# Kernel optimization log

Hardware: AMD Instinct MI355X
Metric: run time of the kernel (lower is better)

## Reference

```python
import jax, jax.numpy as jnp
import numpy as np

EPS = 1e-8
LAM = 0.7  # resonance_lambda


def phase_resonance(a, b, eps=EPS):
    # a, b: (B, N, D) float32. Pairwise phase coherence -> (B, N, N)
    D = a.shape[-1]
    pairs = (D // 2)
    a2 = a[..., :pairs * 2].reshape(*a.shape[:-1], pairs, 2)
    b2 = b[..., :pairs * 2].reshape(*b.shape[:-1], pairs, 2)
    theta_a = jnp.arctan2(a2[..., 1] + eps, a2[..., 0] + eps)  # (B,N,pairs)
    theta_b = jnp.arctan2(b2[..., 1] + eps, b2[..., 0] + eps)  # (B,N,pairs)
    delta = theta_a[:, :, None, :] - theta_b[:, None, :, :]    # (B,N,N,pairs)
    return jnp.cos(delta).mean(axis=-1)                        # (B,N,N)


def setup_inputs() -> dict:
    key = jax.random.key(0)
    k1, k2, k3, k4, k5 = jax.random.split(key, 5)
    B, N, D = 2, 1024, 128
    node_states = jax.random.normal(k1, (B, N, D), dtype=jnp.float32)
    node_gates = jax.random.uniform(k2, (B, N, 1), dtype=jnp.float32)
    r_acc = jax.random.normal(k3, (B, N, N), dtype=jnp.float32)
    # nn.Linear(D, D, bias=False) weights, y = x @ W.T
    scale = 1.0 / np.sqrt(D)
    W_in = jax.random.uniform(k4, (D, D), dtype=jnp.float32, minval=-scale, maxval=scale)
    W_out = jax.random.uniform(k5, (D, D), dtype=jnp.float32, minval=-scale, maxval=scale)
    conductance = jnp.asarray(1.0, dtype=jnp.float32)
    return {"node_states": node_states, "node_gates": node_gates, "r_acc": r_acc,
            "W_in": W_in, "W_out": W_out, "conductance": conductance}


def reference(node_states, node_gates, r_acc, W_in, W_out, conductance):
    B, N, D = node_states.shape
    h = node_states @ W_in.T                                   # field_in projection
    r_instant = phase_resonance(h, h)                          # (B,N,N)
    r_acc_new = LAM * r_acc + (1.0 - LAM) * r_instant
    r_acc_new = jnp.clip(r_acc_new, -2.0, 2.0)
    cond = jnp.clip(conductance, -5.0, 5.0)
    coupling = jax.nn.sigmoid(cond * r_acc_new)                # (B,N,N)
    eye = jnp.eye(N, dtype=coupling.dtype)[None]               # zero self-coupling
    coupling = coupling * (1.0 - eye)
    coupling = coupling * jnp.swapaxes(node_gates, -1, -2)     # (B,1,N) col gates
    coupling = coupling * node_gates                           # (B,N,1) row gates
    coupling = coupling / (coupling.sum(axis=-1, keepdims=True) + 1e-8)
    transmitted = node_states * node_gates
    values = transmitted @ W_out.T                             # field_out projection
    field_signal = coupling @ values                           # (B,N,D)
    return field_signal, r_acc_new
```

## Files before the change

### kernel.cpp

```cpp
#include <hip/hip_runtime.h>
#include <hip/hip_bf16.h>

using bf16x8 = __attribute__((ext_vector_type(8))) short;
using f32x4  = __attribute__((ext_vector_type(4))) float;

#define NN 1024
#define DD 128

__global__ void init_kernel(float* __restrict__ rowsum) {
    int i = blockIdx.x * 256 + threadIdx.x;
    if (i < 2 * NN) rowsum[i] = 0.0f;
}

__global__ __launch_bounds__(256) void prep_kernel(
    const float* __restrict__ states, const float* __restrict__ gates,
    const float* __restrict__ W_in, const float* __restrict__ W_out,
    __hip_bfloat16* __restrict__ M_bf, __hip_bfloat16* __restrict__ valT)
{
    __shared__ float s_state[4 * 128];
    __shared__ float s_WinT[32 * 129];
    __shared__ float s_WoutT[32 * 129];
    __shared__ float s_g[4];

    const int tid = threadIdx.x;
    const int b  = blockIdx.x >> 8;
    const int n0 = (blockIdx.x & 255) * 4;

    const float* sb = states + ((size_t)b * NN + n0) * DD;
    if (tid < 128) ((float4*)s_state)[tid] = ((const float4*)sb)[tid];
    if (tid < 4)   s_g[tid] = gates[b * NN + n0 + tid];

    const int c  = tid & 127;
    const int rg = tid >> 7;
    float acc_h[2] = {0.f, 0.f};
    float acc_v[2] = {0.f, 0.f};

    const int kk = tid & 31;
    const int dg = tid >> 5;
    for (int k0 = 0; k0 < 128; k0 += 32) {
        __syncthreads();
        #pragma unroll
        for (int dd = 0; dd < 16; ++dd) {
            int d = dg * 16 + dd;
            s_WinT [kk * 129 + d] = W_in [d * 128 + k0 + kk];
            s_WoutT[kk * 129 + d] = W_out[d * 128 + k0 + kk];
        }
        __syncthreads();
        #pragma unroll
        for (int k2 = 0; k2 < 32; ++k2) {
            float w1 = s_WinT [k2 * 129 + c];
            float w2 = s_WoutT[k2 * 129 + c];
            #pragma unroll
            for (int r = 0; r < 2; ++r) {
                float s = s_state[(rg * 2 + r) * 128 + k0 + k2];
                acc_h[r] = fmaf(s, w1, acc_h[r]);
                acc_v[r] = fmaf(s, w2, acc_v[r]);
            }
        }
    }

    #pragma unroll
    for (int r = 0; r < 2; ++r) {
        int row = rg * 2 + r;
        float hm = acc_h[r] + 1e-8f;
        float hp = __shfl_xor(hm, 1);
        float x = (c & 1) ? hp : hm;
        float y = (c & 1) ? hm : hp;
        float r2 = x * x + y * y;
        float out;
        if (r2 > 0.f) out = ((c & 1) ? y : x) * rsqrtf(r2);
        else          out = (c & 1) ? 0.f : 1.f;
        M_bf[((size_t)b * NN + n0 + row) * DD + c] = __float2bfloat16(out);
        valT[((size_t)b * DD + c) * NN + n0 + row] = __float2bfloat16(acc_v[r] * s_g[row]);
    }
}

__global__ __launch_bounds__(256) void resonance_kernel(
    const __hip_bfloat16* __restrict__ M_bf,
    const float* __restrict__ r_acc,
    const float* __restrict__ gates,
    const float* __restrict__ cond_ptr,
    float* __restrict__ r_out,
    __hip_bfloat16* __restrict__ c_bf,
    float* __restrict__ rowsum)
{
    const int tid = threadIdx.x;
    const int l  = tid & 63;
    const int w  = tid >> 6;
    const int j0 = blockIdx.x * 32;
    const int i0 = blockIdx.y * 64;
    const int b  = blockIdx.z;

    const int row_a = l & 15;
    const int kg    = l >> 4;

    const bf16x8* Mv = (const bf16x8*)(M_bf + (size_t)b * NN * DD);

    f32x4 acc[2];
    #pragma unroll
    for (int cp = 0; cp < 2; ++cp) acc[cp] = (f32x4){0.f, 0.f, 0.f, 0.f};

    #pragma unroll
    for (int ks = 0; ks < 4; ++ks) {
        int kv = ks * 4 + kg;
        bf16x8 a = Mv[(size_t)(i0 + w * 16 + row_a) * 16 + kv];
        #pragma unroll
        for (int cp = 0; cp < 2; ++cp) {
            bf16x8 bb = Mv[(size_t)(j0 + cp * 16 + row_a) * 16 + kv];
            acc[cp] = __builtin_amdgcn_mfma_f32_16x16x32_bf16(a, bb, acc[cp], 0, 0, 0);
        }
    }

    float cond = fminf(fmaxf(cond_ptr[0], -5.f), 5.f);
    const int i_base = i0 + w * 16 + kg * 4;

    float g_j[2], g_i[4];
    #pragma unroll
    for (int cp = 0; cp < 2; ++cp) g_j[cp] = gates[b * NN + j0 + cp * 16 + row_a];
    #pragma unroll
    for (int q = 0; q < 4; ++q)    g_i[q]  = gates[b * NN + i_base + q];

    const size_t robase = (size_t)b * NN * NN;
    float rs[4] = {0.f, 0.f, 0.f, 0.f};

    #pragma unroll
    for (int q = 0; q < 4; ++q) {
        int i = i_base + q;
        float gi = g_i[q];
        #pragma unroll
        for (int cp = 0; cp < 2; ++cp) {
            int j = j0 + cp * 16 + row_a;
            float s  = acc[cp][q] * (1.f / 64.f);
            float ra = r_acc[robase + (size_t)i * NN + j];
            float rn = fminf(fmaxf(0.7f * ra + 0.3f * s, -2.f), 2.f);
            r_out[robase + (size_t)i * NN + j] = rn;
            float cpl = (i == j) ? 0.f
                        : (1.f / (1.f + __expf(-cond * rn))) * gi * g_j[cp];
            c_bf[robase + (size_t)i * NN + j] = __float2bfloat16(cpl);
            rs[q] += cpl;
        }
    }

    #pragma unroll
    for (int q = 0; q < 4; ++q) {
        float v = rs[q];
        v += __shfl_xor(v, 1);
        v += __shfl_xor(v, 2);
        v += __shfl_xor(v, 4);
        v += __shfl_xor(v, 8);
        if ((l & 15) == 0) atomicAdd(&rowsum[b * NN + i_base + q], v);
    }
}

__global__ __launch_bounds__(256) void gather_kernel(
    const __hip_bfloat16* __restrict__ c_bf,
    const __hip_bfloat16* __restrict__ valT,
    __hip_bfloat16* __restrict__ part)
{
    const int tid = threadIdx.x;
    const int l  = tid & 63;
    const int w  = tid >> 6;
    const int jc = blockIdx.x;
    const int i0 = blockIdx.y * 64;
    const int b  = blockIdx.z;

    const int row_a = l & 15;
    const int kg    = l >> 4;

    const bf16x8* Cv = (const bf16x8*)(c_bf + (size_t)b * NN * NN);
    const bf16x8* Vv = (const bf16x8*)(valT + (size_t)b * DD * NN);

    f32x4 acc[8];
    #pragma unroll
    for (int dt = 0; dt < 8; ++dt) acc[dt] = (f32x4){0.f, 0.f, 0.f, 0.f};

    #pragma unroll
    for (int s = 0; s < 2; ++s) {
        int kv = jc * 8 + s * 4 + kg;
        bf16x8 a = Cv[(size_t)(i0 + w * 16 + row_a) * (NN / 8) + kv];
        #pragma unroll
        for (int dt = 0; dt < 8; ++dt) {
            bf16x8 bb = Vv[(size_t)(dt * 16 + row_a) * (NN / 8) + kv];
            acc[dt] = __builtin_amdgcn_mfma_f32_16x16x32_bf16(a, bb, acc[dt], 0, 0, 0);
        }
    }

    __hip_bfloat16* pb = part + ((size_t)jc * 2 + b) * NN * DD;
    #pragma unroll
    for (int dt = 0; dt < 8; ++dt) {
        #pragma unroll
        for (int q = 0; q < 4; ++q) {
            int i = i0 + w * 16 + kg * 4 + q;
            int d = dt * 16 + row_a;
            pb[(size_t)i * DD + d] = __float2bfloat16(acc[dt][q]);
        }
    }
}

__global__ __launch_bounds__(256) void reduce_kernel(
    const __hip_bfloat16* __restrict__ part,
    const float* __restrict__ rowsum,
    float* __restrict__ field)
{
    int p   = blockIdx.x * 256 + threadIdx.x;
    int b   = p >> 16;
    int rem = p & 65535;
    int i   = rem >> 6;
    int d2  = (rem & 63) * 2;
    size_t base = ((size_t)b * NN + i) * DD + d2;

    float s0 = 0.f, s1 = 0.f;
    #pragma unroll
    for (int jc = 0; jc < 16; ++jc) {
        unsigned int u = *(const unsigned int*)(part + (size_t)jc * 2 * NN * DD + base);
        s0 += __uint_as_float(u << 16);
        s1 += __uint_as_float(u & 0xffff0000u);
    }
    float inv = 1.0f / (rowsum[b * NN + i] + 1e-8f);
    float2 o = {s0 * inv, s1 * inv};
    *(float2*)(field + base) = o;
}

extern "C" void kernel_launch(void* const* d_in, const int* in_sizes, int n_in,
                              void* d_out, int out_size, void* d_ws, size_t ws_size,
                              hipStream_t stream) {
    const float* states = (const float*)d_in[0];
    const float* gates  = (const float*)d_in[1];
    const float* r_acc  = (const float*)d_in[2];
    const float* W_in   = (const float*)d_in[3];
    const float* W_out  = (const float*)d_in[4];
    const float* cond   = (const float*)d_in[5];

    float* field = (float*)d_out;
    float* r_out = field + 2 * NN * DD;

    char* ws = (char*)d_ws;
    __hip_bfloat16* M_bf   = (__hip_bfloat16*)ws;
    __hip_bfloat16* valT   = (__hip_bfloat16*)(ws + (512 << 10));
    __hip_bfloat16* c_bf   = (__hip_bfloat16*)(ws + (1 << 20));
    float*          rowsum = (float*)(ws + (5 << 20));
    __hip_bfloat16* part   = (__hip_bfloat16*)(ws + (6 << 20));

    hipLaunchKernelGGL(init_kernel, dim3(8), dim3(256), 0, stream, rowsum);
    hipLaunchKernelGGL(prep_kernel, dim3(512), dim3(256), 0, stream,
                       states, gates, W_in, W_out, M_bf, valT);
    hipLaunchKernelGGL(resonance_kernel, dim3(32, 16, 2), dim3(256), 0, stream,
                       M_bf, r_acc, gates, cond, r_out, c_bf, rowsum);
    hipLaunchKernelGGL(gather_kernel, dim3(16, 16, 2), dim3(256), 0, stream,
                       c_bf, valT, part);
    hipLaunchKernelGGL(reduce_kernel, dim3(512), dim3(256), 0, stream,
                       part, rowsum, field);
}
```

Baseline: 110.6 us.

## Fuse resonance and gather kernels via shared-memory coupling tile, drop atomics

```diff
diff --git a/kernel.cpp b/kernel.cpp
--- a/kernel.cpp
+++ b/kernel.cpp
@@ -2,14 +2,15 @@
 #include <hip/hip_bf16.h>
 
 using bf16x8 = __attribute__((ext_vector_type(8))) short;
+using bf16x4 = __attribute__((ext_vector_type(4))) short;
 using f32x4  = __attribute__((ext_vector_type(4))) float;
 
 #define NN 1024
 #define DD 128
 
-__global__ void init_kernel(float* __restrict__ rowsum) {
-    int i = blockIdx.x * 256 + threadIdx.x;
-    if (i < 2 * NN) rowsum[i] = 0.0f;
+__device__ __forceinline__ short bf16bits(float f) {
+    __hip_bfloat16 t = __float2bfloat16(f);
+    return *(short*)&t;
 }
 
 __global__ __launch_bounds__(256) void prep_kernel(
@@ -20,6 +21,7 @@
     __shared__ float s_state[4 * 128];
     __shared__ float s_WinT[32 * 129];
     __shared__ float s_WoutT[32 * 129];
+    __shared__ float s_v[4][128];
     __shared__ float s_g[4];
 
     const int tid = threadIdx.x;
@@ -35,15 +37,23 @@
     float acc_h[2] = {0.f, 0.f};
     float acc_v[2] = {0.f, 0.f};
 
-    const int kk = tid & 31;
-    const int dg = tid >> 5;
+    const int kq = tid & 7;
+    const int dl = tid >> 3;
     for (int k0 = 0; k0 < 128; k0 += 32) {
         __syncthreads();
         #pragma unroll
-        for (int dd = 0; dd < 16; ++dd) {
-            int d = dg * 16 + dd;
-            s_WinT [kk * 129 + d] = W_in [d * 128 + k0 + kk];
-            s_WoutT[kk * 129 + d] = W_out[d * 128 + k0 + kk];
+        for (int dp = 0; dp < 4; ++dp) {
+            int d = dp * 32 + dl;
+            float4 w1 = *(const float4*)(W_in  + d * 128 + k0 + kq * 4);
+            float4 w2 = *(const float4*)(W_out + d * 128 + k0 + kq * 4);
+            s_WinT [(kq * 4 + 0) * 129 + d] = w1.x;
+            s_WinT [(kq * 4 + 1) * 129 + d] = w1.y;
+            s_WinT [(kq * 4 + 2) * 129 + d] = w1.z;
+            s_WinT [(kq * 4 + 3) * 129 + d] = w1.w;
+            s_WoutT[(kq * 4 + 0) * 129 + d] = w2.x;
+            s_WoutT[(kq * 4 + 1) * 129 + d] = w2.y;
+            s_WoutT[(kq * 4 + 2) * 129 + d] = w2.z;
+            s_WoutT[(kq * 4 + 3) * 129 + d] = w2.w;
         }
         __syncthreads();
         #pragma unroll
@@ -71,52 +81,67 @@
         if (r2 > 0.f) out = ((c & 1) ? y : x) * rsqrtf(r2);
         else          out = (c & 1) ? 0.f : 1.f;
         M_bf[((size_t)b * NN + n0 + row) * DD + c] = __float2bfloat16(out);
-        valT[((size_t)b * DD + c) * NN + n0 + row] = __float2bfloat16(acc_v[r] * s_g[row]);
-    }
-}
-
-__global__ __launch_bounds__(256) void resonance_kernel(
+        s_v[row][c] = acc_v[r] * s_g[row];
+    }
+    __syncthreads();
+
+    if (tid < 128) {
+        bf16x4 pk;
+        #pragma unroll
+        for (int r = 0; r < 4; ++r) pk[r] = bf16bits(s_v[r][tid]);
+        *(bf16x4*)(valT + ((size_t)b * DD + tid) * NN + n0) = pk;
+    }
+}
+
+__global__ __launch_bounds__(256) void fused_kernel(
     const __hip_bfloat16* __restrict__ M_bf,
+    const __hip_bfloat16* __restrict__ valT,
     const float* __restrict__ r_acc,
     const float* __restrict__ gates,
     const float* __restrict__ cond_ptr,
     float* __restrict__ r_out,
-    __hip_bfloat16* __restrict__ c_bf,
-    float* __restrict__ rowsum)
+    __hip_bfloat16* __restrict__ part,
+    float* __restrict__ part_rs)
 {
+    __shared__ __align__(16) __hip_bfloat16 s_cpl[2][16][72];
+    __shared__ float s_rs[32][2];
+
     const int tid = threadIdx.x;
     const int l  = tid & 63;
     const int w  = tid >> 6;
-    const int j0 = blockIdx.x * 32;
-    const int i0 = blockIdx.y * 64;
-    const int b  = blockIdx.z;
-
+    const int wi = w & 1;
+    const int wj = w >> 1;
     const int row_a = l & 15;
     const int kg    = l >> 4;
 
+    const int jt = blockIdx.x;
+    const int j0 = jt * 64;
+    const int i0 = blockIdx.y * 32;
+    const int b  = blockIdx.z;
+
     const bf16x8* Mv = (const bf16x8*)(M_bf + (size_t)b * NN * DD);
+    const bf16x8* Vv = (const bf16x8*)(valT + (size_t)b * DD * NN);
 
     f32x4 acc[2];
-    #pragma unroll
-    for (int cp = 0; cp < 2; ++cp) acc[cp] = (f32x4){0.f, 0.f, 0.f, 0.f};
-
+    acc[0] = (f32x4){0.f, 0.f, 0.f, 0.f};
+    acc[1] = (f32x4){0.f, 0.f, 0.f, 0.f};
     #pragma unroll
     for (int ks = 0; ks < 4; ++ks) {
         int kv = ks * 4 + kg;
-        bf16x8 a = Mv[(size_t)(i0 + w * 16 + row_a) * 16 + kv];
+        bf16x8 a = Mv[(size_t)(i0 + wi * 16 + row_a) * 16 + kv];
         #pragma unroll
         for (int cp = 0; cp < 2; ++cp) {
-            bf16x8 bb = Mv[(size_t)(j0 + cp * 16 + row_a) * 16 + kv];
+            bf16x8 bb = Mv[(size_t)(j0 + wj * 32 + cp * 16 + row_a) * 16 + kv];
             acc[cp] = __builtin_amdgcn_mfma_f32_16x16x32_bf16(a, bb, acc[cp], 0, 0, 0);
         }
     }
 
     float cond = fminf(fmaxf(cond_ptr[0], -5.f), 5.f);
-    const int i_base = i0 + w * 16 + kg * 4;
+    const int i_base = i0 + wi * 16 + kg * 4;
 
     float g_j[2], g_i[4];
     #pragma unroll
-    for (int cp = 0; cp < 2; ++cp) g_j[cp] = gates[b * NN + j0 + cp * 16 + row_a];
+    for (int cp = 0; cp < 2; ++cp) g_j[cp] = gates[b * NN + j0 + wj * 32 + cp * 16 + row_a];
     #pragma unroll
     for (int q = 0; q < 4; ++q)    g_i[q]  = gates[b * NN + i_base + q];
 
@@ -129,15 +154,16 @@
         float gi = g_i[q];
         #pragma unroll
         for (int cp = 0; cp < 2; ++cp) {
-            int j = j0 + cp * 16 + row_a;
+            int jl = wj * 32 + cp * 16 + row_a;
+            int j  = j0 + jl;
             float s  = acc[cp][q] * (1.f / 64.f);
             float ra = r_acc[robase + (size_t)i * NN + j];
             float rn = fminf(fmaxf(0.7f * ra + 0.3f * s, -2.f), 2.f);
             r_out[robase + (size_t)i * NN + j] = rn;
             float cpl = (i == j) ? 0.f
                         : (1.f / (1.f + __expf(-cond * rn))) * gi * g_j[cp];
-            c_bf[robase + (size_t)i * NN + j] = __float2bfloat16(cpl);
             rs[q] += cpl;
+            s_cpl[wi][kg * 4 + q][jl] = __float2bfloat16(cpl);
         }
     }
 
@@ -148,77 +174,66 @@
         v += __shfl_xor(v, 2);
         v += __shfl_xor(v, 4);
         v += __shfl_xor(v, 8);
-        if ((l & 15) == 0) atomicAdd(&rowsum[b * NN + i_base + q], v);
-    }
-}
-
-__global__ __launch_bounds__(256) void gather_kernel(
-    const __hip_bfloat16* __restrict__ c_bf,
-    const __hip_bfloat16* __restrict__ valT,
-    __hip_bfloat16* __restrict__ part)
-{
-    const int tid = threadIdx.x;
-    const int l  = tid & 63;
-    const int w  = tid >> 6;
-    const int jc = blockIdx.x;
-    const int i0 = blockIdx.y * 64;
-    const int b  = blockIdx.z;
-
-    const int row_a = l & 15;
-    const int kg    = l >> 4;
-
-    const bf16x8* Cv = (const bf16x8*)(c_bf + (size_t)b * NN * NN);
-    const bf16x8* Vv = (const bf16x8*)(valT + (size_t)b * DD * NN);
-
-    f32x4 acc[8];
-    #pragma unroll
-    for (int dt = 0; dt < 8; ++dt) acc[dt] = (f32x4){0.f, 0.f, 0.f, 0.f};
-
-    #pragma unroll
-    for (int s = 0; s < 2; ++s) {
-        int kv = jc * 8 + s * 4 + kg;
-        bf16x8 a = Cv[(size_t)(i0 + w * 16 + row_a) * (NN / 8) + kv];
-        #pragma unroll
-        for (int dt = 0; dt < 8; ++dt) {
-            bf16x8 bb = Vv[(size_t)(dt * 16 + row_a) * (NN / 8) + kv];
-            acc[dt] = __builtin_amdgcn_mfma_f32_16x16x32_bf16(a, bb, acc[dt], 0, 0, 0);
-        }
-    }
-
-    __hip_bfloat16* pb = part + ((size_t)jc * 2 + b) * NN * DD;
-    #pragma unroll
-    for (int dt = 0; dt < 8; ++dt) {
+        if (row_a == 0) s_rs[wi * 16 + kg * 4 + q][wj] = v;
+    }
+    __syncthreads();
+
+    f32x4 pacc[4];
+    #pragma unroll
+    for (int dt = 0; dt < 4; ++dt) pacc[dt] = (f32x4){0.f, 0.f, 0.f, 0.f};
+
+    #pragma unroll
+    for (int ks2 = 0; ks2 < 2; ++ks2) {
+        bf16x8 a = *(const bf16x8*)&s_cpl[wi][row_a][ks2 * 32 + kg * 8];
+        #pragma unroll
+        for (int dt = 0; dt < 4; ++dt) {
+            int d = (wj * 4 + dt) * 16 + row_a;
+            bf16x8 bb = Vv[(size_t)d * (NN / 8) + (j0 >> 3) + ks2 * 4 + kg];
+            pacc[dt] = __builtin_amdgcn_mfma_f32_16x16x32_bf16(a, bb, pacc[dt], 0, 0, 0);
+        }
+    }
+
+    __hip_bfloat16* pb = part + ((size_t)jt * 2 + b) * NN * DD;
+    #pragma unroll
+    for (int dt = 0; dt < 4; ++dt) {
         #pragma unroll
         for (int q = 0; q < 4; ++q) {
-            int i = i0 + w * 16 + kg * 4 + q;
-            int d = dt * 16 + row_a;
-            pb[(size_t)i * DD + d] = __float2bfloat16(acc[dt][q]);
-        }
-    }
+            int i = i0 + wi * 16 + kg * 4 + q;
+            int d = (wj * 4 + dt) * 16 + row_a;
+            pb[(size_t)i * DD + d] = __float2bfloat16(pacc[dt][q]);
+        }
+    }
+
+    if (tid < 32)
+        part_rs[((size_t)jt * 2 + b) * NN + i0 + tid] = s_rs[tid][0] + s_rs[tid][1];
 }
 
 __global__ __launch_bounds__(256) void reduce_kernel(
     const __hip_bfloat16* __restrict__ part,
-    const float* __restrict__ rowsum,
+    const float* __restrict__ part_rs,
     float* __restrict__ field)
 {
-    int p   = blockIdx.x * 256 + threadIdx.x;
-    int b   = p >> 16;
-    int rem = p & 65535;
-    int i   = rem >> 6;
-    int d2  = (rem & 63) * 2;
-    size_t base = ((size_t)b * NN + i) * DD + d2;
-
-    float s0 = 0.f, s1 = 0.f;
-    #pragma unroll
-    for (int jc = 0; jc < 16; ++jc) {
-        unsigned int u = *(const unsigned int*)(part + (size_t)jc * 2 * NN * DD + base);
-        s0 += __uint_as_float(u << 16);
-        s1 += __uint_as_float(u & 0xffff0000u);
-    }
-    float inv = 1.0f / (rowsum[b * NN + i] + 1e-8f);
-    float2 o = {s0 * inv, s1 * inv};
-    *(float2*)(field + base) = o;
+    int t   = blockIdx.x * 256 + threadIdx.x;
+    int b   = t >> 15;
+    int rem = t & 32767;
+    int i   = rem >> 5;
+    int d4  = (rem & 31) * 4;
+    size_t ibase = (size_t)i * DD + d4;
+
+    float s0 = 0.f, s1 = 0.f, s2 = 0.f, s3 = 0.f, rsum = 0.f;
+    #pragma unroll
+    for (int jt = 0; jt < 16; ++jt) {
+        size_t slab = ((size_t)jt * 2 + b);
+        uint2 u = *(const uint2*)(part + slab * NN * DD + ibase);
+        s0 += __uint_as_float(u.x << 16);
+        s1 += __uint_as_float(u.x & 0xffff0000u);
+        s2 += __uint_as_float(u.y << 16);
+        s3 += __uint_as_float(u.y & 0xffff0000u);
+        rsum += part_rs[slab * NN + i];
+    }
+    float inv = 1.0f / (rsum + 1e-8f);
+    float4 o = {s0 * inv, s1 * inv, s2 * inv, s3 * inv};
+    *(float4*)(field + ((size_t)b * NN + i) * DD + d4) = o;
 }
 
 extern "C" void kernel_launch(void* const* d_in, const int* in_sizes, int n_in,
@@ -235,19 +250,15 @@
     float* r_out = field + 2 * NN * DD;
 
     char* ws = (char*)d_ws;
-    __hip_bfloat16* M_bf   = (__hip_bfloat16*)ws;
-    __hip_bfloat16* valT   = (__hip_bfloat16*)(ws + (512 << 10));
-    __hip_bfloat16* c_bf   = (__hip_bfloat16*)(ws + (1 << 20));
-    float*          rowsum = (float*)(ws + (5 << 20));
-    __hip_bfloat16* part   = (__hip_bfloat16*)(ws + (6 << 20));
-
-    hipLaunchKernelGGL(init_kernel, dim3(8), dim3(256), 0, stream, rowsum);
+    __hip_bfloat16* M_bf    = (__hip_bfloat16*)ws;
+    __hip_bfloat16* valT    = (__hip_bfloat16*)(ws + (512 << 10));
+    __hip_bfloat16* part    = (__hip_bfloat16*)(ws + (1 << 20));
+    float*          part_rs = (float*)(ws + (9 << 20));
+
     hipLaunchKernelGGL(prep_kernel, dim3(512), dim3(256), 0, stream,
                        states, gates, W_in, W_out, M_bf, valT);
-    hipLaunchKernelGGL(resonance_kernel, dim3(32, 16, 2), dim3(256), 0, stream,
-                       M_bf, r_acc, gates, cond, r_out, c_bf, rowsum);
-    hipLaunchKernelGGL(gather_kernel, dim3(16, 16, 2), dim3(256), 0, stream,
-                       c_bf, valT, part);
-    hipLaunchKernelGGL(reduce_kernel, dim3(512), dim3(256), 0, stream,
-                       part, rowsum, field);
-}
+    hipLaunchKernelGGL(fused_kernel, dim3(16, 32, 2), dim3(256), 0, stream,
+                       M_bf, valT, r_acc, gates, cond, r_out, part, part_rs);
+    hipLaunchKernelGGL(reduce_kernel, dim3(256), dim3(256), 0, stream,
+                       part, part_rs, field);
+}
```

Result: faster. 101.1 us (-8.5%).
